# Kernel tuning notes

Measured on AMD Instinct MI355X. Metric: run time of the kernel, lower is better.

Reference implementation:

```python
import jax, jax.numpy as jnp
import numpy as np

B, L, D, K = 16, 2048, 768, 32
NEG = jnp.float32(-1e30)

def setup_inputs() -> dict:
    key = jax.random.key(0)
    k1, k2, k3, k4 = jax.random.split(key, 4)
    token_hidden = jax.random.normal(k1, (B, L, D), dtype=jnp.float32)
    attention_mask = jnp.ones((B, L), dtype=jnp.float32)
    # ragged spans: sorted boundaries -> contiguous, possibly-empty spans
    bounds = jnp.sort(jax.random.randint(k2, (B, K + 1), 0, L), axis=-1)
    span_starts = bounds[:, :-1].astype(jnp.int32)   # [B, K]
    span_ends = bounds[:, 1:].astype(jnp.int32)      # [B, K]
    w_pool = jax.random.normal(k3, (D,), dtype=jnp.float32) * 0.02
    b_pool = jax.random.normal(k4, (1,), dtype=jnp.float32) * 0.02
    return {"token_hidden": token_hidden, "attention_mask": attention_mask,
            "span_starts": span_starts, "span_ends": span_ends,
            "w_pool": w_pool, "b_pool": b_pool}

def reference(token_hidden, attention_mask, span_starts, span_ends, w_pool, b_pool):
    # sent_pool(vecs): scores per token, shared across spans  -> [B, L]
    scores = jnp.einsum('bld,d->bl', token_hidden, w_pool) + b_pool[0]
    pos = jnp.arange(token_hidden.shape[1], dtype=jnp.int32)  # [L]
    # span membership mask [B, K, L]; empty / out-of-range spans -> all False
    span_mask = ((pos[None, None, :] >= span_starts[:, :, None]) &
                 (pos[None, None, :] < span_ends[:, :, None]) &
                 (attention_mask[:, None, :] >= 0.5))
    logits = jnp.where(span_mask, scores[:, None, :], NEG)  # [B, K, L]
    m = jnp.max(logits, axis=-1, keepdims=True)
    e = jnp.exp(logits - m) * span_mask                      # stable masked softmax
    s = jnp.sum(e, axis=-1, keepdims=True)
    w = e / jnp.maximum(s, jnp.float32(1e-30))               # zero rows for empty spans
    H = jnp.einsum('bkl,bld->bkd', w, token_hidden)          # [B, K, D]
    sent_mask = jnp.any(span_mask, axis=-1).astype(jnp.float32)  # [B, K]
    return H, sent_mask
```

## Files before the change

kernel.cpp:

```cpp
#include <hip/hip_runtime.h>

#define BB 16
#define LL 2048
#define DD 768
#define KK 32
#define JJ 4
#define AW 4
#define SLOTS (JJ * AW)

__global__ __launch_bounds__(256) void span_wsum_f(
    const float* __restrict__ th,
    const float* __restrict__ attn,
    const int* __restrict__ sps,
    const int* __restrict__ spe,
    const float* __restrict__ wp,
    float* __restrict__ pacc,
    float* __restrict__ psum) {
  const int bk = blockIdx.x;
  const int j  = blockIdx.y;
  const int b  = bk >> 5;
  const int t    = threadIdx.x;
  const int lane = t & 63;
  const int wave = t >> 6;
  const int slot = j * AW + wave;

  __shared__ float sacc[AW][DD];
  __shared__ float ssum[AW];

  const int s0 = min(max(sps[bk], 0), LL);
  const int e0 = min(max(spe[bk], 0), LL);

  const float4* wr = (const float4*)wp;
  const float4 w0 = wr[lane], w1 = wr[lane + 64], w2 = wr[lane + 128];

  const float* arow = attn + (size_t)b * LL;
  const float4* tb  = (const float4*)(th + (size_t)b * LL * DD);

  float s = 0.f;
  float4 a0 = make_float4(0.f, 0.f, 0.f, 0.f), a1 = a0, a2 = a0;

  #pragma unroll 4
  for (int l = s0 + slot; l < e0; l += SLOTS) {
    const float4* row = tb + (size_t)l * (DD / 4);
    float4 r0 = row[lane], r1 = row[lane + 64], r2 = row[lane + 128];
    const float am = arow[l];

    float d = 0.f;
    d = fmaf(r0.x, w0.x, d); d = fmaf(r0.y, w0.y, d);
    d = fmaf(r0.z, w0.z, d); d = fmaf(r0.w, w0.w, d);
    d = fmaf(r1.x, w1.x, d); d = fmaf(r1.y, w1.y, d);
    d = fmaf(r1.z, w1.z, d); d = fmaf(r1.w, w1.w, d);
    d = fmaf(r2.x, w2.x, d); d = fmaf(r2.y, w2.y, d);
    d = fmaf(r2.z, w2.z, d); d = fmaf(r2.w, w2.w, d);
    #pragma unroll
    for (int o = 32; o > 0; o >>= 1) d += __shfl_xor(d, o, 64);

    float e = __expf(d);
    e = (am >= 0.5f) ? e : 0.f;
    s += e;
    a0.x = fmaf(e, r0.x, a0.x); a0.y = fmaf(e, r0.y, a0.y);
    a0.z = fmaf(e, r0.z, a0.z); a0.w = fmaf(e, r0.w, a0.w);
    a1.x = fmaf(e, r1.x, a1.x); a1.y = fmaf(e, r1.y, a1.y);
    a1.z = fmaf(e, r1.z, a1.z); a1.w = fmaf(e, r1.w, a1.w);
    a2.x = fmaf(e, r2.x, a2.x); a2.y = fmaf(e, r2.y, a2.y);
    a2.z = fmaf(e, r2.z, a2.z); a2.w = fmaf(e, r2.w, a2.w);
  }

  float4* sa = (float4*)sacc[wave];
  sa[lane] = a0; sa[lane + 64] = a1; sa[lane + 128] = a2;
  if (lane == 0) ssum[wave] = s;
  __syncthreads();

  if (t < DD / 4) {
    float4 o = make_float4(0.f, 0.f, 0.f, 0.f);
    #pragma unroll
    for (int w = 0; w < AW; ++w) {
      const float4 p = ((const float4*)sacc[w])[t];
      o.x += p.x; o.y += p.y; o.z += p.z; o.w += p.w;
    }
    ((float4*)(pacc + (size_t)(bk * JJ + j) * DD))[t] = o;
  }
  if (t == 0) psum[bk * JJ + j] = ssum[0] + ssum[1] + ssum[2] + ssum[3];
}

__global__ __launch_bounds__(192) void span_merge(
    const float* __restrict__ pacc,
    const float* __restrict__ psum,
    float* __restrict__ Hout,
    float* __restrict__ sent) {
  const int bk = blockIdx.x;
  const int t = threadIdx.x;

  float S = 0.f;
  #pragma unroll
  for (int jv = 0; jv < JJ; ++jv) S += psum[bk * JJ + jv];
  const float inv = (S > 0.f) ? (1.0f / S) : 0.f;

  float4 o = make_float4(0.f, 0.f, 0.f, 0.f);
  #pragma unroll
  for (int jv = 0; jv < JJ; ++jv) {
    const float4 p = ((const float4*)(pacc + (size_t)(bk * JJ + jv) * DD))[t];
    o.x += p.x; o.y += p.y; o.z += p.z; o.w += p.w;
  }
  o.x *= inv; o.y *= inv; o.z *= inv; o.w *= inv;
  ((float4*)(Hout + (size_t)bk * DD))[t] = o;
  if (t == 0) sent[bk] = (S > 0.f) ? 1.0f : 0.0f;
}

extern "C" void kernel_launch(void* const* d_in, const int* in_sizes, int n_in,
                              void* d_out, int out_size, void* d_ws, size_t ws_size,
                              hipStream_t stream) {
  const float* th   = (const float*)d_in[0];
  const float* attn = (const float*)d_in[1];
  const int*   sps  = (const int*)d_in[2];
  const int*   spe  = (const int*)d_in[3];
  const float* wp   = (const float*)d_in[4];

  float* Hout = (float*)d_out;
  float* sent = Hout + (size_t)BB * KK * DD;

  float* pacc = (float*)d_ws;
  float* psum = pacc + (size_t)BB * KK * JJ * DD;

  span_wsum_f<<<dim3(BB * KK, JJ), dim3(256), 0, stream>>>(
      th, attn, sps, spe, wp, pacc, psum);
  span_merge<<<dim3(BB * KK), dim3(192), 0, stream>>>(
      pacc, psum, Hout, sent);
}
```

Baseline: 175.4 us.

## Load-balance ragged spans via a prefix-sum chunk schedule and atomic accumulation

A single-block scheduler kernel takes the prefix sum of per-span chunk counts, with 64 tokens per chunk, and writes a work table. A fixed grid of 1024 blocks of 512 threads then processes one chunk each, so work follows the ragged span lengths instead of giving every span a fixed number of blocks. Partial sums go into a zeroed workspace through float atomics, and a final kernel normalizes. This adds two extra launches, a serial scheduler block and atomic traffic. It also assumes the total chunk count fits within 1024 and makes the summation order nondeterministic.

New measurement: 167.2 us. 1.05x faster.

```diff
diff --git a/kernel.cpp b/kernel.cpp
--- a/kernel.cpp
+++ b/kernel.cpp
@@ -4,66 +4,102 @@
 #define LL 2048
 #define DD 768
 #define KK 32
-#define JJ 4
-#define AW 4
-#define SLOTS (JJ * AW)
+#define NSPAN (BB * KK)
+#define CH 64
+#define MAXCHUNK 1024
+#define CW 8
 
-__global__ __launch_bounds__(256) void span_wsum_f(
+
+__global__ __launch_bounds__(256) void zero_ws(float* __restrict__ p, int n) {
+  int i = blockIdx.x * 256 + threadIdx.x;
+  const int stride = gridDim.x * 256;
+  for (; i < n; i += stride) p[i] = 0.f;
+}
+
+__global__ __launch_bounds__(512) void sched_k(
+    const int* __restrict__ sps, const int* __restrict__ spe,
+    int* __restrict__ table, int* __restrict__ cnt) {
+  __shared__ int cs[NSPAN];
+  const int t = threadIdx.x;
+  const int s0 = min(max(sps[t], 0), LL);
+  const int e0 = min(max(spe[t], 0), LL);
+  const int len = max(e0 - s0, 0);
+  const int c = (len + CH - 1) / CH;
+  cs[t] = c;
+  __syncthreads();
+  #pragma unroll
+  for (int off = 1; off < NSPAN; off <<= 1) {
+    const int v = (t >= off) ? cs[t - off] : 0;
+    __syncthreads();
+    cs[t] += v;
+    __syncthreads();
+  }
+  const int base = cs[t] - c;
+  for (int i = 0; i < c; ++i) table[base + i] = (t << 6) | i;
+  if (t == NSPAN - 1) *cnt = cs[t];
+}
+
+__global__ __launch_bounds__(512) void span_chunk(
     const float* __restrict__ th,
     const float* __restrict__ attn,
     const int* __restrict__ sps,
     const int* __restrict__ spe,
     const float* __restrict__ wp,
+    const int* __restrict__ table,
+    const int* __restrict__ cnt,
     float* __restrict__ pacc,
-    float* __restrict__ psum) {
-  const int bk = blockIdx.x;
-  const int j  = blockIdx.y;
+    float* __restrict__ S) {
+  const int id = blockIdx.x;
+  if (id >= *cnt) return;
+  const int entry = table[id];
+  const int bk = entry >> 6;
+  const int c  = entry & 63;
   const int b  = bk >> 5;
-  const int t    = threadIdx.x;
-  const int lane = t & 63;
-  const int wave = t >> 6;
-  const int slot = j * AW + wave;
+  const int t = threadIdx.x, lane = t & 63, wave = t >> 6;
 
-  __shared__ float sacc[AW][DD];
-  __shared__ float ssum[AW];
+  __shared__ float sacc[CW][DD];
+  __shared__ float ssum[CW];
 
   const int s0 = min(max(sps[bk], 0), LL);
   const int e0 = min(max(spe[bk], 0), LL);
+  const int r0 = s0 + c * CH;
+  const int r1 = min(r0 + CH, e0);
 
   const float4* wr = (const float4*)wp;
   const float4 w0 = wr[lane], w1 = wr[lane + 64], w2 = wr[lane + 128];
-
   const float* arow = attn + (size_t)b * LL;
   const float4* tb  = (const float4*)(th + (size_t)b * LL * DD);
 
   float s = 0.f;
   float4 a0 = make_float4(0.f, 0.f, 0.f, 0.f), a1 = a0, a2 = a0;
 
-  #pragma unroll 4
-  for (int l = s0 + slot; l < e0; l += SLOTS) {
+  const int wr0 = r0 + wave * (CH / CW);
+  const int wr1 = min(wr0 + CH / CW, r1);
+  #pragma unroll 2
+  for (int l = wr0; l < wr1; ++l) {
     const float4* row = tb + (size_t)l * (DD / 4);
-    float4 r0 = row[lane], r1 = row[lane + 64], r2 = row[lane + 128];
+    float4 r0v = row[lane], r1v = row[lane + 64], r2v = row[lane + 128];
     const float am = arow[l];
 
     float d = 0.f;
-    d = fmaf(r0.x, w0.x, d); d = fmaf(r0.y, w0.y, d);
-    d = fmaf(r0.z, w0.z, d); d = fmaf(r0.w, w0.w, d);
-    d = fmaf(r1.x, w1.x, d); d = fmaf(r1.y, w1.y, d);
-    d = fmaf(r1.z, w1.z, d); d = fmaf(r1.w, w1.w, d);
-    d = fmaf(r2.x, w2.x, d); d = fmaf(r2.y, w2.y, d);
-    d = fmaf(r2.z, w2.z, d); d = fmaf(r2.w, w2.w, d);
+    d = fmaf(r0v.x, w0.x, d); d = fmaf(r0v.y, w0.y, d);
+    d = fmaf(r0v.z, w0.z, d); d = fmaf(r0v.w, w0.w, d);
+    d = fmaf(r1v.x, w1.x, d); d = fmaf(r1v.y, w1.y, d);
+    d = fmaf(r1v.z, w1.z, d); d = fmaf(r1v.w, w1.w, d);
+    d = fmaf(r2v.x, w2.x, d); d = fmaf(r2v.y, w2.y, d);
+    d = fmaf(r2v.z, w2.z, d); d = fmaf(r2v.w, w2.w, d);
     #pragma unroll
     for (int o = 32; o > 0; o >>= 1) d += __shfl_xor(d, o, 64);
 
     float e = __expf(d);
     e = (am >= 0.5f) ? e : 0.f;
     s += e;
-    a0.x = fmaf(e, r0.x, a0.x); a0.y = fmaf(e, r0.y, a0.y);
-    a0.z = fmaf(e, r0.z, a0.z); a0.w = fmaf(e, r0.w, a0.w);
-    a1.x = fmaf(e, r1.x, a1.x); a1.y = fmaf(e, r1.y, a1.y);
-    a1.z = fmaf(e, r1.z, a1.z); a1.w = fmaf(e, r1.w, a1.w);
-    a2.x = fmaf(e, r2.x, a2.x); a2.y = fmaf(e, r2.y, a2.y);
-    a2.z = fmaf(e, r2.z, a2.z); a2.w = fmaf(e, r2.w, a2.w);
+    a0.x = fmaf(e, r0v.x, a0.x); a0.y = fmaf(e, r0v.y, a0.y);
+    a0.z = fmaf(e, r0v.z, a0.z); a0.w = fmaf(e, r0v.w, a0.w);
+    a1.x = fmaf(e, r1v.x, a1.x); a1.y = fmaf(e, r1v.y, a1.y);
+    a1.z = fmaf(e, r1v.z, a1.z); a1.w = fmaf(e, r1v.w, a1.w);
+    a2.x = fmaf(e, r2v.x, a2.x); a2.y = fmaf(e, r2v.y, a2.y);
+    a2.z = fmaf(e, r2v.z, a2.z); a2.w = fmaf(e, r2v.w, a2.w);
   }
 
   float4* sa = (float4*)sacc[wave];
@@ -74,37 +110,33 @@
   if (t < DD / 4) {
     float4 o = make_float4(0.f, 0.f, 0.f, 0.f);
     #pragma unroll
-    for (int w = 0; w < AW; ++w) {
+    for (int w = 0; w < CW; ++w) {
       const float4 p = ((const float4*)sacc[w])[t];
       o.x += p.x; o.y += p.y; o.z += p.z; o.w += p.w;
     }
-    ((float4*)(pacc + (size_t)(bk * JJ + j) * DD))[t] = o;
+    float* dst = pacc + (size_t)bk * DD + t * 4;
+    atomicAdd(dst + 0, o.x); atomicAdd(dst + 1, o.y);
+    atomicAdd(dst + 2, o.z); atomicAdd(dst + 3, o.w);
   }
-  if (t == 0) psum[bk * JJ + j] = ssum[0] + ssum[1] + ssum[2] + ssum[3];
+  if (t == 0) {
+    float st = 0.f;
+    #pragma unroll
+    for (int w = 0; w < CW; ++w) st += ssum[w];
+    atomicAdd(&S[bk], st);
+  }
 }
 
-__global__ __launch_bounds__(192) void span_merge(
-    const float* __restrict__ pacc,
-    const float* __restrict__ psum,
-    float* __restrict__ Hout,
-    float* __restrict__ sent) {
+__global__ __launch_bounds__(192) void norm_k(
+    const float* __restrict__ pacc, const float* __restrict__ S,
+    float* __restrict__ Hout, float* __restrict__ sent) {
   const int bk = blockIdx.x;
   const int t = threadIdx.x;
-
-  float S = 0.f;
-  #pragma unroll
-  for (int jv = 0; jv < JJ; ++jv) S += psum[bk * JJ + jv];
-  const float inv = (S > 0.f) ? (1.0f / S) : 0.f;
-
-  float4 o = make_float4(0.f, 0.f, 0.f, 0.f);
-  #pragma unroll
-  for (int jv = 0; jv < JJ; ++jv) {
-    const float4 p = ((const float4*)(pacc + (size_t)(bk * JJ + jv) * DD))[t];
-    o.x += p.x; o.y += p.y; o.z += p.z; o.w += p.w;
-  }
-  o.x *= inv; o.y *= inv; o.z *= inv; o.w *= inv;
-  ((float4*)(Hout + (size_t)bk * DD))[t] = o;
-  if (t == 0) sent[bk] = (S > 0.f) ? 1.0f : 0.0f;
+  const float sv = S[bk];
+  const float inv = (sv > 0.f) ? (1.0f / sv) : 0.f;
+  float4 p = ((const float4*)(pacc + (size_t)bk * DD))[t];
+  p.x *= inv; p.y *= inv; p.z *= inv; p.w *= inv;
+  ((float4*)(Hout + (size_t)bk * DD))[t] = p;
+  if (t == 0) sent[bk] = (sv > 0.f) ? 1.0f : 0.0f;
 }
 
 extern "C" void kernel_launch(void* const* d_in, const int* in_sizes, int n_in,
@@ -119,11 +151,14 @@
   float* Hout = (float*)d_out;
   float* sent = Hout + (size_t)BB * KK * DD;
 
-  float* pacc = (float*)d_ws;
-  float* psum = pacc + (size_t)BB * KK * JJ * DD;
+  float* pacc  = (float*)d_ws;
+  float* Sacc  = pacc + (size_t)NSPAN * DD;
+  int*   table = (int*)(Sacc + NSPAN);
+  int*   cnt   = table + MAXCHUNK;
 
-  span_wsum_f<<<dim3(BB * KK, JJ), dim3(256), 0, stream>>>(
-      th, attn, sps, spe, wp, pacc, psum);
-  span_merge<<<dim3(BB * KK), dim3(192), 0, stream>>>(
-      pacc, psum, Hout, sent);
+  zero_ws<<<dim3(512), dim3(256), 0, stream>>>(pacc, NSPAN * DD + NSPAN);
+  sched_k<<<dim3(1), dim3(512), 0, stream>>>(sps, spe, table, cnt);
+  span_chunk<<<dim3(MAXCHUNK), dim3(512), 0, stream>>>(
+      th, attn, sps, spe, wp, table, cnt, pacc, Sacc);
+  norm_k<<<dim3(NSPAN), dim3(192), 0, stream>>>(pacc, Sacc, Hout, sent);
 }
```
